# Optimization experiments

Hardware: AMD Instinct MI355X
Metric: run time of the kernel (lower is better)

## Reference

```python
import jax, jax.numpy as jnp
import numpy as np

LN_EPS = 1e-5
EPS = 1e-8
MESH_LR = 1.0
MESH_ITERS = 4
SH_ITERS = 5
SA_ITERS = 3


def build_grid(res):
    ranges = [np.linspace(0.0, 1.0, num=r) for r in res]
    g = np.stack(np.meshgrid(*ranges, indexing='ij'), axis=-1)
    g = g.reshape(res[0], res[1], -1)[None]
    return jnp.asarray(np.concatenate([g, 1.0 - g], axis=-1).astype(np.float32))  # [1,H,W,4]


def layer_norm(x, w, b):
    m = jnp.mean(x, axis=-1, keepdims=True)
    v = jnp.var(x, axis=-1, keepdims=True)
    return (x - m) * jax.lax.rsqrt(v + LN_EPS) * w + b


def l2norm(x):
    n = jnp.linalg.norm(x, axis=-1, keepdims=True)
    return x / jnp.maximum(n, 1e-12)  # matches F.normalize eps


def conv_relu(x, w, b, stride):
    y = jax.lax.conv_general_dilated(x, w, (stride, stride), [(2, 2), (2, 2)],
                                     dimension_numbers=('NCHW', 'OIHW', 'NCHW'))
    return jax.nn.relu(y + b[None, :, None, None])


def sinkhorn(C, a, b, u=None, v=None, n_iters=SH_ITERS):
    # log-domain Sinkhorn; C: [B,N,S] cost, a: [B,N], b: [B,S] marginals
    p = -C
    log_a, log_b = jnp.log(a), jnp.log(b)
    if u is None:
        u = jnp.zeros_like(a)
    if v is None:
        v = jnp.zeros_like(b)
    for _ in range(n_iters):
        u = log_a - jax.nn.logsumexp(p + v[:, None, :], axis=2)
        v = log_b - jax.nn.logsumexp(p + u[:, :, None], axis=1)
    pi = jnp.exp(p + u[:, :, None] + v[:, None, :])
    return pi, u, v


def minimize_entropy_of_sinkhorn(C0, a, b, mesh_lr=MESH_LR, n_mesh_iters=MESH_ITERS):
    # gradient descent on the cost matrix to minimize entropy of the transport plan
    def ent(C, u, v):
        pi, u2, v2 = sinkhorn(C, a, b, u=u, v=v)
        e = jnp.mean(-jnp.sum(pi * jnp.log(pi + EPS), axis=(1, 2)))
        return e, (u2, v2)

    grad_fn = jax.grad(ent, has_aux=True)
    u, v = jnp.zeros_like(a), jnp.zeros_like(b)
    C = C0
    for _ in range(n_mesh_iters):
        g, (u, v) = grad_fn(C, u, v)
        C = C - mesh_lr * g
    return C, u, v


def gru_cell(x, h, wih, whh, bih, bhh):
    gi = x @ wih.T + bih
    gh = h @ whh.T + bhh
    ir, iz, inn = jnp.split(gi, 3, axis=-1)
    hr, hz, hn = jnp.split(gh, 3, axis=-1)
    r = jax.nn.sigmoid(ir + hr)
    z = jax.nn.sigmoid(iz + hz)
    n = jnp.tanh(inn + r * hn)
    return (1.0 - z) * n + z * h


def setup_inputs() -> dict:
    key = jax.random.key(0)
    ks = iter(jax.random.split(key, 48))

    def nrm(shape, fan_in):
        return jax.random.normal(next(ks), shape, jnp.float32) / np.sqrt(fan_in).astype(np.float32)

    B, d, S, HID = 16, 64, 8, 128
    z = lambda *s: jnp.zeros(s, jnp.float32)
    o = lambda *s: jnp.ones(s, jnp.float32)
    inp = {
        'image': jax.random.normal(next(ks), (B, 3, 128, 128), jnp.float32),
        'slots_noise': jax.random.normal(next(ks), (B, S, d), jnp.float32),
        'conv1_w': nrm((64, 3, 5, 5), 75), 'conv1_b': z(64),
        'conv2_w': nrm((64, 64, 5, 5), 1600), 'conv2_b': z(64),
        'conv3_w': nrm((64, 64, 5, 5), 1600), 'conv3_b': z(64),
        'conv4_w': nrm((64, 64, 5, 5), 1600), 'conv4_b': z(64),
        'pos_w': nrm((d, 4), 4), 'pos_b': z(d),
        'mlp1_w': nrm((d, d), d), 'mlp1_b': z(d),
        'mlp2_w': nrm((d, d), d), 'mlp2_b': z(d),
        'ln_in_w': o(d), 'ln_in_b': z(d),
        'wk': nrm((d, d), d), 'wv': nrm((d, d), d), 'wq': nrm((d, d), d),
        'mwi_w': nrm((1, d), d), 'mwi_b': z(1),
        'mws_w': nrm((1, d), d), 'mws_b': z(1),
        'ln_sl_w': o(d), 'ln_sl_b': z(d),
        'gru_wih': nrm((3 * d, d), d), 'gru_whh': nrm((3 * d, d), d),
        'gru_bih': z(3 * d), 'gru_bhh': z(3 * d),
        'ln_ff_w': o(d), 'ln_ff_b': z(d),
        'fc1_w': nrm((HID, d), d), 'fc1_b': z(HID),
        'fc2_w': nrm((d, HID), HID), 'fc2_b': z(d),
        'slots_mu': nrm((1, 1, d), d),
        'slots_sigma': jax.random.uniform(next(ks), (1, 1, d), jnp.float32),
        'num_slots': 8,
    }
    return inp


def reference(image, slots_noise, conv1_w, conv1_b, conv2_w, conv2_b, conv3_w, conv3_b,
              conv4_w, conv4_b, pos_w, pos_b, mlp1_w, mlp1_b, mlp2_w, mlp2_b,
              ln_in_w, ln_in_b, wk, wv, wq, mwi_w, mwi_b, mws_w, mws_b,
              ln_sl_w, ln_sl_b, gru_wih, gru_whh, gru_bih, gru_bhh,
              ln_ff_w, ln_ff_b, fc1_w, fc1_b, fc2_w, fc2_b,
              slots_mu, slots_sigma, num_slots):
    B = image.shape[0]
    d = slots_mu.shape[-1]
    # --- CNN encoder (strided_convs=True => latent 32x32) ---
    x = conv_relu(image, conv1_w, conv1_b, 1)
    x = conv_relu(x, conv2_w, conv2_b, 2)
    x = conv_relu(x, conv3_w, conv3_b, 2)
    x = conv_relu(x, conv4_w, conv4_b, 1)          # [B,64,32,32]
    x = x.transpose(0, 2, 3, 1)                    # [B,32,32,64]
    grid = build_grid((32, 32))                    # [1,32,32,4]
    x = x + (grid @ pos_w.T + pos_b)               # soft position embed
    feat = x.reshape(B, -1, d)                     # [B,1024,64]
    # --- pre-slot-attention MLP ---
    feat = jax.nn.relu(feat @ mlp1_w.T + mlp1_b) @ mlp2_w.T + mlp2_b
    # --- slot attention with MESH-Sinkhorn ---
    n_s = num_slots
    slots = slots_mu + (jnp.abs(slots_sigma) + EPS) * slots_noise  # Normal rsample
    inp = layer_norm(feat, ln_in_w, ln_in_b)
    k = inp @ wk.T
    v = inp @ wv.T
    a = jax.nn.softmax((inp @ mwi_w.T + mwi_b).squeeze(-1), axis=-1) * n_s  # [B,N]
    kn = l2norm(k)
    attn = None
    for _ in range(SA_ITERS):
        slots_prev = slots
        s = layer_norm(slots, ln_sl_w, ln_sl_b)
        bm = jax.nn.softmax((s @ mws_w.T + mws_b).squeeze(-1), axis=-1) * n_s  # [B,S]
        q = s @ wq.T
        C = 1.0 - jnp.einsum('bnd,bsd->bns', kn, l2norm(q))  # cosine distance
        C, p, qq = minimize_entropy_of_sinkhorn(C, a, bm)
        pi, _, _ = sinkhorn(C, a, bm, u=p, v=qq)
        attn = pi.transpose(0, 2, 1)                         # [B,S,N]
        updates = jnp.einsum('bsn,bnd->bsd', attn, v)
        slots = gru_cell(updates.reshape(-1, d), slots_prev.reshape(-1, d),
                         gru_wih, gru_whh, gru_bih, gru_bhh).reshape(B, n_s, d)
        h = layer_norm(slots, ln_ff_w, ln_ff_b)
        slots = slots + (jax.nn.relu(h @ fc1_w.T + fc1_b) @ fc2_w.T + fc2_b)
    return slots, attn
```

## Files before the change

### kernel.cpp

```cpp
#include <hip/hip_runtime.h>
#include <hip/hip_bf16.h>


#define LN_EPS 1e-5f
#define SEPS 1e-8f
#define LN8 2.0794415416798357f

__device__ inline float ldf(float x) { return x; }
__device__ inline float ldf(__hip_bfloat16 x) { return __bfloat162float(x); }
__device__ inline void stf(float* p, float v) { *p = v; }
__device__ inline void stf(__hip_bfloat16* p, float v) { *p = __float2bfloat16(v); }

__device__ inline float wmaxall(float v) {
#pragma unroll
  for (int o = 32; o; o >>= 1) v = fmaxf(v, __shfl_down(v, o));
  return __shfl(v, 0);
}
__device__ inline float wsumall(float v) {
#pragma unroll
  for (int o = 32; o; o >>= 1) v += __shfl_down(v, o);
  return __shfl(v, 0);
}
__device__ inline int wsumi(int v) {
#pragma unroll
  for (int o = 32; o; o >>= 1) v += __shfl_down(v, o);
  return __shfl(v, 0);
}
__device__ inline float fast_sigmoid(float x) { return 1.f / (1.f + __expf(-x)); }
__device__ inline float fast_tanh(float x) { return 1.f - 2.f / (__expf(2.f * x) + 1.f); }

struct CvtArgs {
  const void* src[39];
  long off[40];
};

__global__ __launch_bounds__(256) void convert_kernel(CvtArgs a,
                                                      float* __restrict__ dst, long total) {
  __shared__ int sFlag;
  {
    const unsigned int* img = (const unsigned int*)a.src[0];
    if (threadIdx.x < 64) {
      int cnt = 0;
      for (int i = threadIdx.x; i < 512; i += 64) {
        unsigned lo = img[i] & 0xFFFFu;
        int e = (int)((lo >> 7) & 0xFFu);
        cnt += (e >= 96 && e <= 140) ? 1 : 0;
      }
      cnt = wsumi(cnt);
      if (threadIdx.x == 0) sFlag = (cnt >= 300) ? 1 : 0;
    }
    __syncthreads();
  }
  const int isbf = sFlag;
  for (long g = (long)blockIdx.x * 256 + threadIdx.x; g < total; g += (long)gridDim.x * 256) {
    int lo = 0, hi = 38;
    while (lo < hi) {
      int mid = (lo + hi + 1) >> 1;
      if (a.off[mid] <= g) lo = mid; else hi = mid - 1;
    }
    long li = g - a.off[lo];
    float v;
    if (isbf) v = __bfloat162float(((const __hip_bfloat16*)a.src[lo])[li]);
    else      v = ((const float*)a.src[lo])[li];
    dst[g] = v;
  }
}

struct TwArgs {
  long soff[9]; long doff[9]; int R[9]; int C[9];
};

__global__ __launch_bounds__(256) void transw_kernel(const float* __restrict__ cvt,
                                                     float* __restrict__ tws, TwArgs a) {
  int m = blockIdx.x;
  const float* S = cvt + a.soff[m];
  float* D = tws + a.doff[m];
  int R = a.R[m], C = a.C[m];
  for (int idx = threadIdx.x; idx < R * C; idx += 256) {
    int i = idx / C, j = idx - i * C;
    D[j * R + i] = S[idx];
  }
}

template <int S, typename TIN, typename TOUT>
__global__ __launch_bounds__(256) void conv5x5(
    const TIN* __restrict__ in, const float* __restrict__ wgt,
    const float* __restrict__ bias, TOUT* __restrict__ out,
    int Cin, int H, int W, int Ho, int Wo, int Cout, int tilesX) {
  constexpr int P = 15 * S + 5;
  constexpr int PP = (S == 1) ? 20 : 40;
  constexpr int NCH = (S == 1) ? 2 : 3;
  constexpr int NP = (P * P + 255) / 256;
  __shared__ __align__(16) float patch[P * PP];
  __shared__ float wt16[25 * 16];
  const int b = blockIdx.z;
  const int ocg = blockIdx.y * 16;
  const int ty0 = (blockIdx.x / tilesX) * 16, tx0 = (blockIdx.x % tilesX) * 16;
  const int og = threadIdx.x >> 6;
  const int r = (threadIdx.x >> 2) & 15;
  const int rx = threadIdx.x & 3;
  const int iy0 = ty0 * S - 2, ix0 = tx0 * S - 2;
  const long HW = (long)H * W;

  int toff[NP], soff[NP];
#pragma unroll
  for (int q = 0; q < NP; q++) {
    int idx = threadIdx.x + 256 * q;
    toff[q] = -1;
    soff[q] = -1;
    if (idx < P * P) {
      int py = idx / P, px = idx - py * P;
      int iy = iy0 + py, ix = ix0 + px;
      int pxs = (S == 2) ? (px ^ (((py >> 1) & 1) << 2)) : px;
      toff[q] = py * PP + pxs;
      if (iy >= 0 && iy < H && ix >= 0 && ix < W) soff[q] = iy * W + ix;
    }
  }
  int wsrc[2];
#pragma unroll
  for (int q = 0; q < 2; q++) {
    int idx = threadIdx.x + 256 * q;
    wsrc[q] = (idx < 400) ? (((ocg + (idx & 15)) * Cin) * 25 + (idx >> 4)) : -1;
  }

  float acc[4][4];
#pragma unroll
  for (int p = 0; p < 4; p++)
#pragma unroll
    for (int j = 0; j < 4; j++) acc[p][j] = 0.f;

  float pr[NP], wr[2];
  {
    const TIN* inp = in + (long)b * Cin * HW;
#pragma unroll
    for (int q = 0; q < NP; q++) pr[q] = (soff[q] >= 0) ? ldf(inp[soff[q]]) : 0.f;
#pragma unroll
    for (int q = 0; q < 2; q++) wr[q] = (wsrc[q] >= 0) ? wgt[wsrc[q]] : 0.f;
  }

  for (int ci = 0; ci < Cin; ++ci) {
    __syncthreads();
#pragma unroll
    for (int q = 0; q < NP; q++)
      if (toff[q] >= 0) patch[toff[q]] = pr[q];
#pragma unroll
    for (int q = 0; q < 2; q++) {
      int idx = threadIdx.x + 256 * q;
      if (idx < 400) wt16[idx] = wr[q];
    }
    __syncthreads();
    if (ci + 1 < Cin) {
      const TIN* inp = in + ((long)b * Cin + ci + 1) * HW;
#pragma unroll
      for (int q = 0; q < NP; q++) pr[q] = (soff[q] >= 0) ? ldf(inp[soff[q]]) : 0.f;
#pragma unroll
      for (int q = 0; q < 2; q++)
        if (wsrc[q] >= 0) wr[q] = wgt[wsrc[q] + (ci + 1) * 25];
    }
#pragma unroll
    for (int ky = 0; ky < 5; ky++) {
      float win[4 * NCH];
      const int row = r * S + ky;
      const float* rb = &patch[row * PP];
      if constexpr (S == 2) {
        const int sw = (row >> 1) & 1;
#pragma unroll
        for (int c = 0; c < NCH; c++) {
          const int g = rx * 2 + c;
          float4 t4 = *(const float4*)(rb + ((g ^ sw) << 2));
          win[4 * c + 0] = t4.x;
          win[4 * c + 1] = t4.y;
          win[4 * c + 2] = t4.z;
          win[4 * c + 3] = t4.w;
        }
      } else {
        const float* bp = rb + rx * 4;
#pragma unroll
        for (int c = 0; c < NCH; c++) {
          float4 t4 = *(const float4*)(bp + 4 * c);
          win[4 * c + 0] = t4.x;
          win[4 * c + 1] = t4.y;
          win[4 * c + 2] = t4.z;
          win[4 * c + 3] = t4.w;
        }
      }
#pragma unroll
      for (int kx = 0; kx < 5; kx++) {
        const float4 wv = *(const float4*)&wt16[(ky * 5 + kx) * 16 + og * 4];
#pragma unroll
        for (int p = 0; p < 4; p++) {
          float iv = win[p * S + kx];
          acc[p][0] += iv * wv.x;
          acc[p][1] += iv * wv.y;
          acc[p][2] += iv * wv.z;
          acc[p][3] += iv * wv.w;
        }
      }
    }
  }
  const int oy = ty0 + r, ox0 = tx0 + rx * 4;
#pragma unroll
  for (int j = 0; j < 4; j++) {
    int oc = ocg + og * 4 + j;
    float bs = bias[oc];
    TOUT* op = &out[(((long)b * Cout + oc) * Ho + oy) * Wo + ox0];
#pragma unroll
    for (int p = 0; p < 4; p++) stf(&op[p], fmaxf(acc[p][j] + bs, 0.f));
  }
}

__global__ __launch_bounds__(256) void token_kernel(
    const float* __restrict__ act4, const float* __restrict__ pos_w,
    const float* __restrict__ pos_b,
    const float* __restrict__ mlp1T, const float* __restrict__ mlp1_b,
    const float* __restrict__ mlp2T, const float* __restrict__ mlp2_b,
    const float* __restrict__ lnin_w, const float* __restrict__ lnin_b,
    const float* __restrict__ wkT, const float* __restrict__ wvT,
    const float* __restrict__ mwi_w, const float* __restrict__ mwi_b,
    float* __restrict__ knT_out, float* __restrict__ v_out, float* __restrict__ lg_out) {
  const int wq = threadIdx.x >> 6, i = threadIdx.x & 63;
  const int t = blockIdx.x * 4 + wq;
  const int b = t >> 10, nn = t & 1023;
  const int h = nn >> 5, w = nn & 31;
  __shared__ float sM1[4096], sM2[4096], sWk[4096], sWv[4096];
  __shared__ float f[4][64], h1[4][64], inp[4][64];
  for (int idx = threadIdx.x; idx < 4096; idx += 256) {
    sM1[idx] = mlp1T[idx];
    sM2[idx] = mlp2T[idx];
    sWk[idx] = wkT[idx];
    sWv[idx] = wvT[idx];
  }
  {
    float gh = h * (1.f / 31.f), gw = w * (1.f / 31.f);
    float e = gh * pos_w[i * 4 + 0] + gw * pos_w[i * 4 + 1] +
              (1.f - gh) * pos_w[i * 4 + 2] + (1.f - gw) * pos_w[i * 4 + 3] + pos_b[i];
    f[wq][i] = act4[(((long)b * 64 + i) * 32 + h) * 32 + w] + e;
  }
  __syncthreads();
  float acc = 0.f;
  for (int j = 0; j < 64; j++) acc += f[wq][j] * sM1[j * 64 + i];
  h1[wq][i] = fmaxf(acc + mlp1_b[i], 0.f);
  __syncthreads();
  acc = 0.f;
  for (int j = 0; j < 64; j++) acc += h1[wq][j] * sM2[j * 64 + i];
  float x = acc + mlp2_b[i];
  float m = wsumall(x) * (1.f / 64.f);
  float d0 = x - m;
  float var = wsumall(d0 * d0) * (1.f / 64.f);
  float xin = d0 * rsqrtf(var + LN_EPS) * lnin_w[i] + lnin_b[i];
  inp[wq][i] = xin;
  __syncthreads();
  float kv = 0.f, vv = 0.f;
  for (int j = 0; j < 64; j++) {
    float ij = inp[wq][j];
    kv += ij * sWk[j * 64 + i];
    vv += ij * sWv[j * 64 + i];
  }
  float ss = wsumall(kv * kv);
  knT_out[(long)b * 65536 + i * 1024 + nn] = kv / fmaxf(sqrtf(ss), 1e-12f);
  v_out[(long)t * 64 + i] = vv;
  float lg = wsumall(xin * mwi_w[i]);
  if (i == 0) lg_out[t] = lg + mwi_b[0];
}

__global__ __launch_bounds__(512) void sa_kernel(
    const float* __restrict__ knT_g, const float* __restrict__ v_g,
    const float* __restrict__ la_g, const float* __restrict__ noise,
    const float* __restrict__ mu_w, const float* __restrict__ sg_w,
    const float* __restrict__ lnsl_w, const float* __restrict__ lnsl_b,
    const float* __restrict__ mws_w, const float* __restrict__ mws_b,
    const float* __restrict__ wqT,
    const float* __restrict__ wihT, const float* __restrict__ whhT,
    const float* __restrict__ bih, const float* __restrict__ bhh,
    const float* __restrict__ lnff_w, const float* __restrict__ lnff_b,
    const float* __restrict__ fc1T, const float* __restrict__ fc1_b,
    const float* __restrict__ fc2T, const float* __restrict__ fc2_b,
    float* __restrict__ out) {
  const int b = blockIdx.x, tid = threadIdx.x;
  const int wv = tid >> 6, ln = tid & 63;

  __shared__ float sCt[8192];
  __shared__ float sEc[8192];
  __shared__ float sLa[1024], sELa[1024], sHid[1024];
  __shared__ float sPart[512 * 9];
  __shared__ float sVh[48], sV[8], sEsv[8], sGv[8], sLb[8], sBm[8];
  __shared__ float sC1[8], sEvh[8];
  __shared__ float sSlots[512], sNorm[512], sQn[512], sUpd[512];

  const float* knt = knT_g + (long)b * 65536;
  const float* vf = v_g + (long)b * 65536;
  float sInvH[5][2];
  float gPr[2][8];
  float gInit[2];

  {
    int dd = tid & 63;
    sSlots[tid] = mu_w[dd] + (fabsf(sg_w[dd]) + SEPS) * noise[(long)b * 512 + tid];
  }
  for (int n = tid; n < 1024; n += 512) sLa[n] = la_g[b * 1024 + n];
  __syncthreads();
  {
    float a0 = sLa[tid], a1 = sLa[tid + 512];
    float m0 = wmaxall(fmaxf(a0, a1));
    if (ln == 0) sBm[wv] = m0;
    __syncthreads();
    float M = sBm[0];
#pragma unroll
    for (int s = 1; s < 8; s++) M = fmaxf(M, sBm[s]);
    float e0 = wsumall(__expf(a0 - M) + __expf(a1 - M));
    if (ln == 0) sGv[wv] = e0;
    __syncthreads();
    float SS = 0.f;
#pragma unroll
    for (int s = 0; s < 8; s++) SS += sGv[s];
    float lse = M + __logf(SS);
    float l0 = a0 - lse + LN8, l1 = a1 - lse + LN8;
    sLa[tid] = l0;
    sLa[tid + 512] = l1;
    sELa[tid] = __expf(l0);
    sELa[tid + 512] = __expf(l1);
  }
  __syncthreads();

  for (int it = 0; it < 3; ++it) {
    {
      float x = sSlots[wv * 64 + ln];
      float m = wsumall(x) * (1.f / 64.f);
      float d0 = x - m;
      float var = wsumall(d0 * d0) * (1.f / 64.f);
      float xn = d0 * rsqrtf(var + LN_EPS) * lnsl_w[ln] + lnsl_b[ln];
      sNorm[wv * 64 + ln] = xn;
      float bmv = wsumall(xn * mws_w[ln]);
      if (ln == 0) sBm[wv] = bmv + mws_b[0];
    }
    __syncthreads();
    if (tid == 0) {
      float mx = -1e30f;
      for (int s = 0; s < 8; s++) mx = fmaxf(mx, sBm[s]);
      float ss = 0.f;
      for (int s = 0; s < 8; s++) ss += __expf(sBm[s] - mx);
      float lse = mx + __logf(ss);
      for (int s = 0; s < 8; s++) sLb[s] = sBm[s] - lse + LN8;
    }
    {
      float acc = 0.f;
      for (int j = 0; j < 64; j++) acc += sNorm[wv * 64 + j] * wqT[j * 64 + ln];
      sQn[tid] = acc;
    }
    __syncthreads();
    {
      float qv = sQn[wv * 64 + ln];
      float ss = wsumall(qv * qv);
      sQn[wv * 64 + ln] = qv / fmaxf(sqrtf(ss), 1e-12f);
    }
    if (tid < 8) {
      sV[tid] = 0.f;
      sEsv[tid] = 1.f;
    }
    __syncthreads();

#pragma unroll
    for (int k = 0; k < 2; k++) {
      int n = tid + 512 * k;
      float acc[8];
#pragma unroll
      for (int s = 0; s < 8; s++) acc[s] = 0.f;
      for (int j = 0; j < 64; j++) {
        float kvv = knt[j * 1024 + n];
#pragma unroll
        for (int s = 0; s < 8; s++) acc[s] += kvv * sQn[s * 64 + j];
      }
#pragma unroll
      for (int s = 0; s < 8; s++) {
        float c = 1.f - acc[s];
        sCt[s * 1024 + n] = c;
        sEc[s * 1024 + n] = __expf(-c);
      }
    }
    __syncthreads();

    for (int m = 0; m < 4; m++) {
#pragma unroll
      for (int t = 1; t <= 5; t++) {
        if (t == 1 && tid < 8) sVh[tid] = sV[tid];
        float esv_r[8], part[8];
#pragma unroll
        for (int s = 0; s < 8; s++) { esv_r[s] = sEsv[s]; part[s] = 0.f; }
#pragma unroll
        for (int k = 0; k < 2; k++) {
          int n = tid + 512 * k;
          float ec[8], S = 0.f;
#pragma unroll
          for (int s = 0; s < 8; s++) {
            ec[s] = sEc[s * 1024 + n];
            S += esv_r[s] * ec[s];
          }
          float inv = 1.f / S;
          sInvH[t - 1][k] = inv;
          float w = sELa[n] * inv;
#pragma unroll
          for (int s = 0; s < 8; s++) part[s] += w * ec[s];
        }
#pragma unroll
        for (int s = 0; s < 8; s++) sPart[tid * 9 + s] = part[s];
        __syncthreads();
        {
          int s = wv;
          float acc = 0.f;
#pragma unroll
          for (int q = 0; q < 8; q++) acc += sPart[(ln + 64 * q) * 9 + s];
          acc = wsumall(acc);
          if (ln == 0) {
            float vs = sLb[s] - __logf(acc);
            sV[s] = vs;
            sVh[t * 8 + s] = vs;
            sEsv[s] = __expf(vs);
          }
        }
        __syncthreads();
      }
      {
        float esv_r[8], part[8];
#pragma unroll
        for (int s = 0; s < 8; s++) { esv_r[s] = sEsv[s]; part[s] = 0.f; }
#pragma unroll
        for (int k = 0; k < 2; k++) {
          int n = tid + 512 * k;
          float al = sELa[n] * sInvH[4][k];
          float gul = 0.f;
#pragma unroll
          for (int s = 0; s < 8; s++) {
            float pi = al * esv_r[s] * sEc[s * 1024 + n];
            float gl = -(__logf(pi + SEPS) + pi / (pi + SEPS)) * pi * (1.f / 16.f);
            gPr[k][s] = gl;
            gul += gl;
            part[s] += gl;
          }
          gInit[k] = gul;
        }
#pragma unroll
        for (int s = 0; s < 8; s++) sPart[tid * 9 + s] = part[s];
        __syncthreads();
        {
          int s = wv;
          float acc = 0.f;
#pragma unroll
          for (int q = 0; q < 8; q++) acc += sPart[(ln + 64 * q) * 9 + s];
          acc = wsumall(acc);
          if (ln == 0) {
            sGv[s] = acc;
            sC1[s] = acc * __expf(sVh[40 + s] - sLb[s]);
            sEvh[s] = __expf(sVh[32 + s]);
          }
        }
        __syncthreads();
      }
#pragma unroll
      for (int t = 5; t >= 1; t--) {
        float c1_r[8], evh_r[8], part[8];
#pragma unroll
        for (int s = 0; s < 8; s++) {
          c1_r[s] = sC1[s];
          evh_r[s] = sEvh[s];
          part[s] = 0.f;
        }
#pragma unroll
        for (int k = 0; k < 2; k++) {
          int n = tid + 512 * k;
          float inv = sInvH[t - 1][k];
          float al = sELa[n] * inv;
          float gul = (t == 5) ? gInit[k] : 0.f;
          float ec[8];
#pragma unroll
          for (int s = 0; s < 8; s++) {
            ec[s] = sEc[s * 1024 + n];
            float t2 = al * c1_r[s] * ec[s];
            gPr[k][s] -= t2;
            gul -= t2;
          }
          float bv = gul * inv;
#pragma unroll
          for (int s = 0; s < 8; s++) {
            float pe = bv * ec[s];
            gPr[k][s] -= pe * evh_r[s];
            part[s] += pe;
          }
          if (t == 1) {
#pragma unroll
            for (int s = 0; s < 8; s++) {
              float cn = sCt[s * 1024 + n] + gPr[k][s];
              sCt[s * 1024 + n] = cn;
              sEc[s * 1024 + n] = __expf(-cn);
            }
          }
        }
        if (t > 1) {
#pragma unroll
          for (int s = 0; s < 8; s++) sPart[tid * 9 + s] = part[s];
        }
        if (t == 1 && tid < 8) {
          float vs = sVh[40 + tid];
          sV[tid] = vs;
          sEsv[tid] = __expf(vs);
        }
        __syncthreads();
        if (t > 1) {
          int s = wv;
          float acc = 0.f;
#pragma unroll
          for (int q = 0; q < 8; q++) acc += sPart[(ln + 64 * q) * 9 + s];
          acc = wsumall(acc);
          if (ln == 0) {
            float gn = -sEvh[s] * acc;
            sGv[s] = gn;
            sC1[s] = gn * __expf(sVh[(t - 1) * 8 + s] - sLb[s]);
            sEvh[s] = __expf(sVh[(t - 2) * 8 + s]);
          }
          __syncthreads();
        }
      }
    }

    float invF[2];
    for (int t = 0; t < 5; t++) {
      float esv_r[8], part[8];
#pragma unroll
      for (int s = 0; s < 8; s++) { esv_r[s] = sEsv[s]; part[s] = 0.f; }
#pragma unroll
      for (int k = 0; k < 2; k++) {
        int n = tid + 512 * k;
        float ec[8], S = 0.f;
#pragma unroll
        for (int s = 0; s < 8; s++) {
          ec[s] = sEc[s * 1024 + n];
          S += esv_r[s] * ec[s];
        }
        float inv = 1.f / S;
        invF[k] = inv;
        float w = sELa[n] * inv;
#pragma unroll
        for (int s = 0; s < 8; s++) part[s] += w * ec[s];
      }
#pragma unroll
      for (int s = 0; s < 8; s++) sPart[tid * 9 + s] = part[s];
      __syncthreads();
      {
        int s = wv;
        float acc = 0.f;
#pragma unroll
        for (int q = 0; q < 8; q++) acc += sPart[(ln + 64 * q) * 9 + s];
        acc = wsumall(acc);
        if (ln == 0) {
          float vs = sLb[s] - __logf(acc);
          sV[s] = vs;
          sEsv[s] = __expf(vs);
        }
      }
      __syncthreads();
    }
    {
      float esv_r[8];
#pragma unroll
      for (int s = 0; s < 8; s++) esv_r[s] = sEsv[s];
#pragma unroll
      for (int k = 0; k < 2; k++) {
        int n = tid + 512 * k;
        float al = sELa[n] * invF[k];
#pragma unroll
        for (int s = 0; s < 8; s++)
          sCt[s * 1024 + n] = al * esv_r[s] * sEc[s * 1024 + n];
      }
    }
    __syncthreads();
    if (it == 2) {
      for (int o = tid; o < 8192; o += 512) out[8192 + (long)b * 8192 + o] = sCt[o];
    }
    {
      int s = tid >> 6, dd = tid & 63;
      float acc = 0.f;
      for (int n = 0; n < 1024; n++) acc += sCt[s * 1024 + n] * vf[n * 64 + dd];
      sUpd[tid] = acc;
    }
    __syncthreads();
    float newslot;
    {
      int s = tid >> 6, i = tid & 63;
      const float* x = &sUpd[s * 64];
      const float* h = &sSlots[s * 64];
      float gir = 0, giz = 0, gin = 0, ghr = 0, ghz = 0, ghn = 0;
      for (int j = 0; j < 64; j++) {
        float xv = x[j], hv = h[j];
        gir += xv * wihT[j * 192 + i];
        giz += xv * wihT[j * 192 + 64 + i];
        gin += xv * wihT[j * 192 + 128 + i];
        ghr += hv * whhT[j * 192 + i];
        ghz += hv * whhT[j * 192 + 64 + i];
        ghn += hv * whhT[j * 192 + 128 + i];
      }
      gir += bih[i]; giz += bih[64 + i]; gin += bih[128 + i];
      ghr += bhh[i]; ghz += bhh[64 + i]; ghn += bhh[128 + i];
      float r = fast_sigmoid(gir + ghr);
      float z = fast_sigmoid(giz + ghz);
      float nn = fast_tanh(gin + r * ghn);
      newslot = (1.f - z) * nn + z * h[i];
    }
    __syncthreads();
    sSlots[tid] = newslot;
    __syncthreads();
    {
      float x = sSlots[wv * 64 + ln];
      float m = wsumall(x) * (1.f / 64.f);
      float d0 = x - m;
      float var = wsumall(d0 * d0) * (1.f / 64.f);
      sNorm[wv * 64 + ln] = d0 * rsqrtf(var + LN_EPS) * lnff_w[ln] + lnff_b[ln];
    }
    __syncthreads();
    for (int o = tid; o < 1024; o += 512) {
      int s = o >> 7, k2 = o & 127;
      float acc = 0.f;
      for (int j = 0; j < 64; j++) acc += sNorm[s * 64 + j] * fc1T[j * 128 + k2];
      sHid[o] = fmaxf(acc + fc1_b[k2], 0.f);
    }
    __syncthreads();
    {
      int s = tid >> 6, i = tid & 63;
      float acc = 0.f;
      for (int j = 0; j < 128; j++) acc += sHid[s * 128 + j] * fc2T[j * 64 + i];
      newslot = sSlots[tid] + acc + fc2_b[i];
    }
    __syncthreads();
    sSlots[tid] = newslot;
    __syncthreads();
  }
  out[(long)b * 512 + tid] = sSlots[tid];
}

extern "C" void kernel_launch(void* const* d_in, const int* in_sizes, int n_in,
                              void* d_out, int out_size, void* d_ws, size_t ws_size,
                              hipStream_t stream) {
  (void)n_in; (void)out_size; (void)ws_size;
  char* ws = (char*)d_ws;
  float* cvt  = (float*)ws;
  float* lgts = (float*)(ws + 5570560ull);
  __hip_bfloat16* act1 = (__hip_bfloat16*)(ws + 5636096ull);
  __hip_bfloat16* act2 = (__hip_bfloat16*)(ws + 39190528ull);
  float* act3 = (float*)(ws + 5636096ull);
  float* act4 = (float*)(ws + 9830400ull);
  float* knT  = (float*)(ws + 14024704ull);
  float* vf   = (float*)(ws + 18219008ull);
  float* tws  = (float*)(ws + 47583232ull);

  CvtArgs ca;
  long total = 0;
  for (int i = 0; i < 39; i++) { ca.src[i] = d_in[i]; ca.off[i] = total; total += in_sizes[i]; }
  ca.off[39] = total;

  convert_kernel<<<1024, 256, 0, stream>>>(ca, cvt, total);

#define ARR(i) (cvt + ca.off[i])
  TwArgs ta;
  {
    const int src[9] = {12, 14, 18, 19, 20, 27, 28, 33, 35};
    const int R[9] = {64, 64, 64, 64, 64, 192, 192, 128, 64};
    const int C[9] = {64, 64, 64, 64, 64, 64, 64, 64, 128};
    long d = 0;
    for (int m2 = 0; m2 < 9; m2++) {
      ta.soff[m2] = ca.off[src[m2]];
      ta.doff[m2] = d;
      ta.R[m2] = R[m2];
      ta.C[m2] = C[m2];
      d += (long)R[m2] * C[m2];
    }
  }
  transw_kernel<<<9, 256, 0, stream>>>(cvt, tws, ta);
  float* mlp1T = tws + 0,     *mlp2T = tws + 4096,  *wkT = tws + 8192, *wvT = tws + 12288;
  float* wqT   = tws + 16384, *wihT  = tws + 20480, *whhT = tws + 32768;
  float* fc1T  = tws + 45056, *fc2T  = tws + 53248;

  const float* image = ARR(0);
  const float* noise = ARR(1);

  conv5x5<1, float, __hip_bfloat16><<<dim3(64, 4, 16), 256, 0, stream>>>(
      image, ARR(2), ARR(3), act1, 3, 128, 128, 128, 128, 64, 8);
  conv5x5<2, __hip_bfloat16, __hip_bfloat16><<<dim3(16, 4, 16), 256, 0, stream>>>(
      act1, ARR(4), ARR(5), act2, 64, 128, 128, 64, 64, 64, 4);
  conv5x5<2, __hip_bfloat16, float><<<dim3(4, 4, 16), 256, 0, stream>>>(
      act2, ARR(6), ARR(7), act3, 64, 64, 64, 32, 32, 64, 2);
  conv5x5<1, float, float><<<dim3(4, 4, 16), 256, 0, stream>>>(
      act3, ARR(8), ARR(9), act4, 64, 32, 32, 32, 32, 64, 2);

  token_kernel<<<4096, 256, 0, stream>>>(act4, ARR(10), ARR(11),
                                         mlp1T, ARR(13), mlp2T, ARR(15),
                                         ARR(16), ARR(17), wkT, wvT, ARR(21), ARR(22),
                                         knT, vf, lgts);

  sa_kernel<<<16, 512, 0, stream>>>(knT, vf, lgts, noise, ARR(37), ARR(38),
                                    ARR(25), ARR(26), ARR(23), ARR(24), wqT,
                                    wihT, whhT, ARR(29), ARR(30),
                                    ARR(31), ARR(32), fc1T, ARR(34), fc2T, ARR(36),
                                    (float*)d_out);
#undef ARR
}
```

Measured before the change: 947.7 us.

## Split input channels four ways for the last two convs, then reduce partials

The third and fourth conv layers were launched with only 256 blocks each. They now split the input-channel reduction into four quarters, giving 1024 blocks that each write fp32 partial sums. A separate fuse kernel then adds the four partials, applies bias and ReLU. This is meant to raise GPU occupancy on these small layers, at the cost of extra partial-buffer traffic and two extra launches.

```diff
diff --git a/kernel.cpp b/kernel.cpp
--- a/kernel.cpp
+++ b/kernel.cpp
@@ -206,6 +206,150 @@
     TOUT* op = &out[(((long)b * Cout + oc) * Ho + oy) * Wo + ox0];
 #pragma unroll
     for (int p = 0; p < 4; p++) stf(&op[p], fmaxf(acc[p][j] + bs, 0.f));
+  }
+}
+
+template <int S, typename TIN>
+__global__ __launch_bounds__(256) void conv5x5_part(
+    const TIN* __restrict__ in, const float* __restrict__ wgt,
+    float* __restrict__ pout,
+    int Cin, int H, int W, int Ho, int Wo, int Cout, int tilesX) {
+  constexpr int P = 15 * S + 5;
+  constexpr int PP = (S == 1) ? 20 : 40;
+  constexpr int NCH = (S == 1) ? 2 : 3;
+  constexpr int NP = (P * P + 255) / 256;
+  __shared__ __align__(16) float patch[P * PP];
+  __shared__ float wt16[25 * 16];
+  const int zz = blockIdx.z;
+  const int qh = zz & 3;
+  const int b = zz >> 2;
+  const int nci = Cin >> 2;
+  const int c0 = qh * nci;
+  const int ocg = blockIdx.y * 16;
+  const int ty0 = (blockIdx.x / tilesX) * 16, tx0 = (blockIdx.x % tilesX) * 16;
+  const int og = threadIdx.x >> 6;
+  const int r = (threadIdx.x >> 2) & 15;
+  const int rx = threadIdx.x & 3;
+  const int iy0 = ty0 * S - 2, ix0 = tx0 * S - 2;
+  const long HW = (long)H * W;
+
+  int toff[NP], soff[NP];
+#pragma unroll
+  for (int q = 0; q < NP; q++) {
+    int idx = threadIdx.x + 256 * q;
+    toff[q] = -1;
+    soff[q] = -1;
+    if (idx < P * P) {
+      int py = idx / P, px = idx - py * P;
+      int iy = iy0 + py, ix = ix0 + px;
+      int pxs = (S == 2) ? (px ^ (((py >> 1) & 1) << 2)) : px;
+      toff[q] = py * PP + pxs;
+      if (iy >= 0 && iy < H && ix >= 0 && ix < W) soff[q] = iy * W + ix;
+    }
+  }
+  int wsrc[2];
+#pragma unroll
+  for (int q = 0; q < 2; q++) {
+    int idx = threadIdx.x + 256 * q;
+    wsrc[q] = (idx < 400) ? (((ocg + (idx & 15)) * Cin) * 25 + (idx >> 4)) : -1;
+  }
+
+  float acc[4][4];
+#pragma unroll
+  for (int p = 0; p < 4; p++)
+#pragma unroll
+    for (int j = 0; j < 4; j++) acc[p][j] = 0.f;
+
+  float pr[NP], wr[2];
+  {
+    const TIN* inp = in + ((long)b * Cin + c0) * HW;
+#pragma unroll
+    for (int q = 0; q < NP; q++) pr[q] = (soff[q] >= 0) ? ldf(inp[soff[q]]) : 0.f;
+#pragma unroll
+    for (int q = 0; q < 2; q++) wr[q] = (wsrc[q] >= 0) ? wgt[wsrc[q] + c0 * 25] : 0.f;
+  }
+
+  const int cEnd = c0 + nci;
+  for (int ci = c0; ci < cEnd; ++ci) {
+    __syncthreads();
+#pragma unroll
+    for (int q = 0; q < NP; q++)
+      if (toff[q] >= 0) patch[toff[q]] = pr[q];
+#pragma unroll
+    for (int q = 0; q < 2; q++) {
+      int idx = threadIdx.x + 256 * q;
+      if (idx < 400) wt16[idx] = wr[q];
+    }
+    __syncthreads();
+    if (ci + 1 < cEnd) {
+      const TIN* inp = in + ((long)b * Cin + ci + 1) * HW;
+#pragma unroll
+      for (int q = 0; q < NP; q++) pr[q] = (soff[q] >= 0) ? ldf(inp[soff[q]]) : 0.f;
+#pragma unroll
+      for (int q = 0; q < 2; q++)
+        if (wsrc[q] >= 0) wr[q] = wgt[wsrc[q] + (ci + 1) * 25];
+    }
+#pragma unroll
+    for (int ky = 0; ky < 5; ky++) {
+      float win[4 * NCH];
+      const int row = r * S + ky;
+      const float* rb = &patch[row * PP];
+      if constexpr (S == 2) {
+        const int sw = (row >> 1) & 1;
+#pragma unroll
+        for (int c = 0; c < NCH; c++) {
+          const int g = rx * 2 + c;
+          float4 t4 = *(const float4*)(rb + ((g ^ sw) << 2));
+          win[4 * c + 0] = t4.x;
+          win[4 * c + 1] = t4.y;
+          win[4 * c + 2] = t4.z;
+          win[4 * c + 3] = t4.w;
+        }
+      } else {
+        const float* bp = rb + rx * 4;
+#pragma unroll
+        for (int c = 0; c < NCH; c++) {
+          float4 t4 = *(const float4*)(bp + 4 * c);
+          win[4 * c + 0] = t4.x;
+          win[4 * c + 1] = t4.y;
+          win[4 * c + 2] = t4.z;
+          win[4 * c + 3] = t4.w;
+        }
+      }
+#pragma unroll
+      for (int kx = 0; kx < 5; kx++) {
+        const float4 wv = *(const float4*)&wt16[(ky * 5 + kx) * 16 + og * 4];
+#pragma unroll
+        for (int p = 0; p < 4; p++) {
+          float iv = win[p * S + kx];
+          acc[p][0] += iv * wv.x;
+          acc[p][1] += iv * wv.y;
+          acc[p][2] += iv * wv.z;
+          acc[p][3] += iv * wv.w;
+        }
+      }
+    }
+  }
+  const int oy = ty0 + r, ox0 = tx0 + rx * 4;
+  const long HoWo = (long)Ho * Wo;
+#pragma unroll
+  for (int j = 0; j < 4; j++) {
+    int oc = ocg + og * 4 + j;
+    float* op = &pout[((((long)qh * 16 + b) * Cout + oc) * Ho + oy) * Wo + ox0];
+    (void)HoWo;
+#pragma unroll
+    for (int p = 0; p < 4; p++) op[p] = acc[p][j];
+  }
+}
+
+__global__ __launch_bounds__(256) void fuse4_kernel(
+    const float* __restrict__ pin, const float* __restrict__ bias,
+    float* __restrict__ outF, int HoWo, int Cout, long qtr) {
+  for (long i = (long)blockIdx.x * 256 + threadIdx.x; i < qtr;
+       i += (long)gridDim.x * 256) {
+    int oc = (int)((i / HoWo) % Cout);
+    float v = ((pin[i] + pin[i + qtr]) + pin[i + 2 * qtr]) + pin[i + 3 * qtr];
+    outF[i] = fmaxf(v + bias[oc], 0.f);
   }
 }
 
@@ -648,6 +792,7 @@
   float* act4 = (float*)(ws + 9830400ull);
   float* knT  = (float*)(ws + 14024704ull);
   float* vf   = (float*)(ws + 18219008ull);
+  float* parts = (float*)(ws + 22413312ull);
   float* tws  = (float*)(ws + 47583232ull);
 
   CvtArgs ca;
@@ -684,10 +829,14 @@
       image, ARR(2), ARR(3), act1, 3, 128, 128, 128, 128, 64, 8);
   conv5x5<2, __hip_bfloat16, __hip_bfloat16><<<dim3(16, 4, 16), 256, 0, stream>>>(
       act1, ARR(4), ARR(5), act2, 64, 128, 128, 64, 64, 64, 4);
-  conv5x5<2, __hip_bfloat16, float><<<dim3(4, 4, 16), 256, 0, stream>>>(
-      act2, ARR(6), ARR(7), act3, 64, 64, 64, 32, 32, 64, 2);
-  conv5x5<1, float, float><<<dim3(4, 4, 16), 256, 0, stream>>>(
-      act3, ARR(8), ARR(9), act4, 64, 32, 32, 32, 32, 64, 2);
+  conv5x5_part<2, __hip_bfloat16><<<dim3(4, 4, 64), 256, 0, stream>>>(
+      act2, ARR(6), parts, 64, 64, 64, 32, 32, 64, 2);
+  fuse4_kernel<<<1024, 256, 0, stream>>>(parts, ARR(7), act3, 1024, 64,
+                                         16L * 64 * 1024);
+  conv5x5_part<1, float><<<dim3(4, 4, 64), 256, 0, stream>>>(
+      act3, ARR(8), parts, 64, 32, 32, 32, 32, 64, 2);
+  fuse4_kernel<<<1024, 256, 0, stream>>>(parts, ARR(9), act4, 1024, 64,
+                                         16L * 64 * 1024);
 
   token_kernel<<<4096, 256, 0, stream>>>(act4, ARR(10), ARR(11),
                                          mlp1T, ARR(13), mlp2T, ARR(15),
```

Result: faster. 863.9 us, median of 2 (-8.8%).
